# Kernel tuning notes

Measured on AMD Instinct MI355X. Metric: run time of the kernel, lower is better.

## Reference

```python
import jax, jax.numpy as jnp
import numpy as np

B, S, D, K = 16384, 50, 512, 5  # batch, pred_horizon(=steps), dec_units, components_n
H = S  # time_stamp width equals pred_horizon


def setup_inputs() -> dict:
    key = jax.random.key(0)
    ks = jax.random.split(key, 13)
    sc = 0.05
    f32 = jnp.float32
    return {
        "conditions": jax.random.normal(ks[0], (B, S, 3), f32),
        "state_h": jax.random.normal(ks[1], (B, D), f32),
        "state_c": jax.random.normal(ks[2], (B, D), f32),
        # merger LSTM (input = enc_h[D] ++ cond[3])
        "W_m": jax.random.normal(ks[3], (D + 3, 4 * D), f32) * sc,
        "U_m": jax.random.normal(ks[4], (D, 4 * D), f32) * sc,
        "b_m": jnp.zeros((4 * D,), f32),
        # merger MDN heads packed: [alphas|mus_long|sigmas_long|mus_lat|sigmas_lat|rhos]
        "Wh_m": jax.random.normal(ks[5], (D + H, 6 * K), f32) * sc,
        "bh_m": jnp.zeros((6 * K,), f32),
        # yielder LSTM
        "W_y": jax.random.normal(ks[6], (D + 3, 4 * D), f32) * sc,
        "U_y": jax.random.normal(ks[7], (D, 4 * D), f32) * sc,
        "b_y": jnp.zeros((4 * D,), f32),
        # yielder MDN heads packed: [alphas|mus_long|sigmas_long]
        "Wh_y": jax.random.normal(ks[8], (D + H, 3 * K), f32) * sc,
        "bh_y": jnp.zeros((3 * K,), f32),
    }


def _lstm_step(x, h, c, W, U, b):
    # Keras LSTM gate order: i, f, g(cell), o
    z = x @ W + h @ U + b
    i, f, g, o = jnp.split(z, 4, axis=-1)
    c2 = jax.nn.sigmoid(f) * c + jax.nn.sigmoid(i) * jnp.tanh(g)
    h2 = jax.nn.sigmoid(o) * jnp.tanh(c2)
    return h2, c2


def reference(conditions, state_h, state_c, W_m, U_m, b_m, Wh_m, bh_m,
              W_y, U_y, b_y, Wh_y, bh_y):
    # time_stamp[s] = ones in [:s+1] (lower-triangular)
    time_stamp = jnp.tril(jnp.ones((S, H), conditions.dtype))
    enc_h = state_h  # re-fed every step, [B, D]
    # With teacher_percent=1.0 both merger and yielder step conditions are
    # conditions[:, t, :3] at step t (step 0 also uses t=0).
    conds_t = jnp.transpose(conditions, (1, 0, 2))  # [S, B, 3]

    def step(carry, xs):
        h_m, c_m, h_y, c_y = carry
        cond_t, ts = xs  # [B,3], [H]
        x_in = jnp.concatenate([enc_h, cond_t], axis=-1)  # [B, D+3]
        ts_b = jnp.broadcast_to(ts, (h_m.shape[0], H))
        # merger vehicle
        h_m, c_m = _lstm_step(x_in, h_m, c_m, W_m, U_m, b_m)
        feat_m = jnp.concatenate([h_m, ts_b], axis=-1)  # [B, D+H]
        zm = feat_m @ Wh_m + bh_m
        a, ml, sl, mlt, slt, r = jnp.split(zm, 6, axis=-1)
        pm = jnp.concatenate([jax.nn.softmax(a, axis=-1), ml, jnp.exp(sl),
                              mlt, jnp.exp(slt), jnp.tanh(r)], axis=-1)  # [B,30]
        # yielder vehicle
        h_y, c_y = _lstm_step(x_in, h_y, c_y, W_y, U_y, b_y)
        feat_y = jnp.concatenate([h_y, ts_b], axis=-1)
        zy = feat_y @ Wh_y + bh_y
        ay, mly, sly = jnp.split(zy, 3, axis=-1)
        py = jnp.concatenate([jax.nn.softmax(ay, axis=-1), mly, jnp.exp(sly)], axis=-1)  # [B,15]
        return (h_m, c_m, h_y, c_y), (pm, py)

    carry0 = (state_h, state_c, state_h, state_c)
    _, (param_m, param_y) = jax.lax.scan(step, carry0, (conds_t, time_stamp))
    param_m = jnp.transpose(param_m, (1, 0, 2))  # [B, S, 30]
    param_y = jnp.transpose(param_y, (1, 0, 2))  # [B, S, 15]
    return param_m, param_y
```

## Files before the change

### kernel.cpp

```cpp
#include <hip/hip_runtime.h>

typedef __bf16 bf16;
typedef __attribute__((ext_vector_type(8))) __bf16 bf16x8;
typedef __attribute__((ext_vector_type(4))) __bf16 bf16x4;
typedef __attribute__((ext_vector_type(4))) float f32x4;
typedef __attribute__((ext_vector_type(4))) int i32x4;

#define B_TOT 16384
#define SEQ 50
#define DH 512
#define ZW 2048
#define NT 16

#define MFMA16(a, b, c) __builtin_amdgcn_mfma_f32_16x16x32_bf16(a, b, c, 0, 0, 0)

__device__ __forceinline__ float fsigm(float x) {
    return __fdividef(1.0f, 1.0f + __expf(-x));
}
__device__ __forceinline__ float ftanh(float x) {
    float e = __expf(2.0f * x);
    return 1.0f - __fdividef(2.0f, e + 1.0f);
}

__device__ __forceinline__ void gload16(const bf16* g, void* l) {
    __builtin_amdgcn_global_load_lds(
        (const __attribute__((address_space(1))) unsigned int*)g,
        (__attribute__((address_space(3))) unsigned int*)l, 16, 0, 0);
}


__global__ void init_state(const float* __restrict__ sh, const float* __restrict__ sc,
                           bf16* __restrict__ h0m, bf16* __restrict__ h0y,
                           float* __restrict__ cm, float* __restrict__ cy) {
    size_t i = (size_t)blockIdx.x * 256 + threadIdx.x;
    float v = sh[i];
    bf16 hb = (bf16)v;
    h0m[i] = hb;
    h0y[i] = hb;
    float c = sc[i];
    cm[i] = c;
    cy[i] = c;
}

__device__ __forceinline__ int orig_col(int colp) {
    return ((colp >> 4) & 3) * 512 + ((colp >> 6) << 4) + (colp & 15);
}

__global__ void reorder_weights(const float* __restrict__ Um, const float* __restrict__ Uy,
                                const float* __restrict__ Wm, const float* __restrict__ Wy,
                                bf16* __restrict__ UtM, bf16* __restrict__ UtY,
                                bf16* __restrict__ WtM, bf16* __restrict__ WtY) {
    int idx = blockIdx.x * 256 + threadIdx.x;
    int which = idx >> 20;
    int r = idx & ((1 << 20) - 1);
    int colp = r >> 9, k = r & 511;
    int orig = orig_col(colp);
    const float* src = which == 0 ? Um : which == 1 ? Uy : which == 2 ? Wm : Wy;
    bf16* dst = which == 0 ? UtM : which == 1 ? UtY : which == 2 ? WtM : WtY;
    int cb = colp >> 4, fr = colp & 15;
    int kt = k >> 5, fq = (k >> 3) & 3, e = k & 7;
    int lane = fq * 16 + fr;
    dst[(((size_t)(cb * 16 + kt) * 64 + lane) << 3) + e] = (bf16)src[(size_t)k * ZW + orig];
}

__global__ void build_wc2(const float* __restrict__ Wm, const float* __restrict__ Wy,
                          float* __restrict__ Wc2M, float* __restrict__ Wc2Y) {
    int idx = blockIdx.x * 256 + threadIdx.x;
    if (idx >= 2 * 512 * 12) return;
    int which = idx / 6144;
    int r2 = idx % 6144;
    int hcol = r2 / 12, rg = r2 % 12;
    int r = rg >> 2, g = rg & 3;
    const float* src = which ? Wy : Wm;
    float* dst = which ? Wc2Y : Wc2M;
    dst[hcol * 12 + rg] = src[(size_t)(512 + r) * ZW + g * 512 + hcol];
}

__global__ void cond_transpose(const float* __restrict__ cond, float* __restrict__ condT4) {
    int idx = blockIdx.x * 256 + threadIdx.x;
    if (idx >= SEQ * B_TOT) return;
    int t = idx / B_TOT, row = idx % B_TOT;
    const float* s = cond + ((size_t)row * SEQ + t) * 3;
    f32x4 v = {s[0], s[1], s[2], 0.f};
    *(f32x4*)(condT4 + (size_t)idx * 4) = v;
}

__global__ void build_heads(const float* __restrict__ Whm, const float* __restrict__ bhm,
                            const float* __restrict__ Why, const float* __restrict__ bhy,
                            bf16* __restrict__ WhmT, bf16* __restrict__ WhyT,
                            float* __restrict__ tscm, float* __restrict__ tscy) {
    int i = blockIdx.x * 256 + threadIdx.x;
    const int N1 = 32 * 512, N2 = 16 * 512, N3 = SEQ * 32, N4 = SEQ * 16;
    if (i < N1) {
        int n = i >> 9, k = i & 511;
        WhmT[i] = (bf16)(n < 30 ? Whm[k * 30 + n] : 0.f);
    } else if (i < N1 + N2) {
        int j = i - N1;
        int n = j >> 9, k = j & 511;
        WhyT[j] = (bf16)(n < 15 ? Why[k * 15 + n] : 0.f);
    } else if (i < N1 + N2 + N3) {
        int j = i - (N1 + N2);
        int tt = j >> 5, col = j & 31;
        float v = 0.f;
        if (col < 30) {
            v = bhm[col];
            for (int s = 0; s <= tt; ++s) v += Whm[(512 + s) * 30 + col];
        }
        tscm[j] = v;
    } else if (i < N1 + N2 + N3 + N4) {
        int j = i - (N1 + N2 + N3);
        int tt = j >> 4, col = j & 15;
        float v = 0.f;
        if (col < 15) {
            v = bhy[col];
            for (int s = 0; s <= tt; ++s) v += Why[(512 + s) * 15 + col];
        }
        tscy[j] = v;
    }
}


#define FENCE() asm volatile("" ::: "memory")
#define BARRIER()                        \
    do {                                 \
        FENCE();                         \
        __builtin_amdgcn_s_barrier();    \
        FENCE();                         \
    } while (0)
#define WAIT_LGKM0()                                          \
    do {                                                      \
        asm volatile("s_waitcnt lgkmcnt(0)" ::: "memory");    \
        __builtin_amdgcn_sched_barrier(0);                    \
    } while (0)
#define WAIT_VM(n)                                                  \
    do {                                                            \
        asm volatile("s_waitcnt vmcnt(" #n ")" ::: "memory");       \
        __builtin_amdgcn_sched_barrier(0);                          \
    } while (0)

template <int MODE>
__global__ __launch_bounds__(256, 3) void gemm_step(
    const bf16* __restrict__ Am, const bf16* __restrict__ Ay,
    const bf16* __restrict__ BtM, const bf16* __restrict__ BtY,
    const bf16* __restrict__ xwM, const bf16* __restrict__ xwY,
    const float* __restrict__ Wc2M, const float* __restrict__ Wc2Y,
    const float* __restrict__ biasM, const float* __restrict__ biasY,
    float* __restrict__ cM, float* __restrict__ cY,
    bf16* __restrict__ hoM, bf16* __restrict__ hoY,
    bf16* __restrict__ xoM, bf16* __restrict__ xoY,
    const float* __restrict__ condT4, int t) {
    __shared__ bf16 As[3][128][32];

    const int tid = threadIdx.x;
    const int wave = tid >> 6, lane = tid & 63;
    const int brow = blockIdx.x * 128, ncb = blockIdx.y * 128;
    const int bz = blockIdx.z;
    const bf16* A = bz ? Ay : Am;
    const bf16* Bt = bz ? BtY : BtM;

    const int fr = lane & 15, fq = lane >> 4;
    const int wr = wave >> 1, wc = wave & 1;

    const int srow = tid >> 2;
    const int sc8 = (((tid & 3) ^ ((srow >> 1) & 3)) << 3);
    const bf16* Asrc = A + (size_t)(brow + srow) * DH + sc8;
    char* stA = (char*)As + wave * 1024;

    const int cxor = ((fq ^ ((fr >> 1) & 3)) << 4);
    const char* Ard = (char*)As + (wr * 64 + fr) * 64 + cxor;

    const uint64_t bbase =
        (uint64_t)(const char*)Bt + (uint64_t)(blockIdx.y * 8 + wc * 4) * 16384 + lane * 16;

    f32x4 acc[4][4];
#pragma unroll
    for (int m = 0; m < 4; ++m)
#pragma unroll
        for (int n = 0; n < 4; ++n) acc[m][n] = (f32x4){0.f, 0.f, 0.f, 0.f};

    i32x4 bgbuf[2][4];

#define STAGE(slot, kts)                                    \
    do {                                                    \
        const bf16* _s = Asrc + (kts) * 32;                 \
        char* _d = stA + (slot) * 8192;                     \
        gload16(_s, _d);                                    \
        gload16(_s + 64 * DH, _d + 4096);                   \
    } while (0)

#define BGLOAD(bank, kts)                                                        \
    do {                                                                         \
        uint64_t _a = bbase + (uint64_t)(kts) * 1024;                            \
        asm volatile("global_load_dwordx4 %0, %1, off"                          \
                     : "=&v"(bgbuf[bank][0]) : "v"(_a) : "memory");              \
        asm volatile("global_load_dwordx4 %0, %1, off"                          \
                     : "=&v"(bgbuf[bank][1]) : "v"(_a + 16384) : "memory");      \
        asm volatile("global_load_dwordx4 %0, %1, off"                          \
                     : "=&v"(bgbuf[bank][2]) : "v"(_a + 32768) : "memory");      \
        asm volatile("global_load_dwordx4 %0, %1, off"                          \
                     : "=&v"(bgbuf[bank][3]) : "v"(_a + 49152) : "memory");      \
    } while (0)

    BGLOAD(0, 0);
    STAGE(0, 0);
    STAGE(1, 1);
    WAIT_VM(2);
    BARRIER();

#pragma unroll
    for (int kt = 0; kt < NT - 1; ++kt) {
        const int rcur = kt % 3;
        STAGE((kt + 2) % 3, (kt + 2 < NT) ? kt + 2 : NT - 1);
        BGLOAD((kt + 1) & 1, kt + 1);
        bf16x8 af[4];
        {
            const char* _a = Ard + rcur * 8192;
            af[0] = *(const bf16x8*)(_a);
            af[1] = *(const bf16x8*)(_a + 1024);
            af[2] = *(const bf16x8*)(_a + 2048);
            af[3] = *(const bf16x8*)(_a + 3072);
        }
        WAIT_LGKM0();
        WAIT_VM(6);
        __builtin_amdgcn_s_setprio(1);
#pragma unroll
        for (int m = 0; m < 4; ++m)
#pragma unroll
            for (int n = 0; n < 4; ++n)
                acc[m][n] = MFMA16(af[m], __builtin_bit_cast(bf16x8, bgbuf[kt & 1][n]),
                                   acc[m][n]);
        __builtin_amdgcn_s_setprio(0);
        __builtin_amdgcn_sched_barrier(0);
        BARRIER();
    }
    {
        bf16x8 af[4];
        const char* _a = Ard + ((NT - 1) % 3) * 8192;
        af[0] = *(const bf16x8*)(_a);
        af[1] = *(const bf16x8*)(_a + 1024);
        af[2] = *(const bf16x8*)(_a + 2048);
        af[3] = *(const bf16x8*)(_a + 3072);
        WAIT_LGKM0();
        WAIT_VM(0);
        __builtin_amdgcn_s_setprio(1);
#pragma unroll
        for (int m = 0; m < 4; ++m)
#pragma unroll
            for (int n = 0; n < 4; ++n)
                acc[m][n] = MFMA16(af[m], __builtin_bit_cast(bf16x8, bgbuf[(NT - 1) & 1][n]),
                                   acc[m][n]);
        __builtin_amdgcn_s_setprio(0);
        __builtin_amdgcn_sched_barrier(0);
    }

    const int jb = blockIdx.y * 2 + wc;
    const int hcol = jb * 16 + fr;
    const int rowbase = brow + wr * 64 + fq * 4;

    if (MODE == 0) {
        const float* bias = bz ? biasY : biasM;
        bf16* XO = bz ? xoY : xoM;
#pragma unroll
        for (int m = 0; m < 4; ++m)
#pragma unroll
            for (int j = 0; j < 4; ++j) {
                const int row = rowbase + m * 16 + j;
                bf16x4 v;
#pragma unroll
                for (int n = 0; n < 4; ++n) v[n] = (bf16)(acc[m][n][j] + bias[n * 512 + hcol]);
                *(bf16x4*)(XO + (size_t)row * ZW + hcol * 4) = v;
            }
    } else {
        float* Cb = bz ? cY : cM;
        bf16* Ho = bz ? hoY : hoM;
        const bf16* xw = bz ? xwY : xwM;
        const float* Wc2 = bz ? Wc2Y : Wc2M;
        f32x4 wcv0 = *(const f32x4*)(Wc2 + hcol * 12);
        f32x4 wcv1 = *(const f32x4*)(Wc2 + hcol * 12 + 4);
        f32x4 wcv2 = *(const f32x4*)(Wc2 + hcol * 12 + 8);
        bf16x4 xwv[4][4];
        float cv[4][4];
#pragma unroll
        for (int m = 0; m < 4; ++m)
#pragma unroll
            for (int j = 0; j < 4; ++j) {
                const int row = rowbase + m * 16 + j;
                xwv[m][j] = *(const bf16x4*)(xw + (size_t)row * ZW + hcol * 4);
                cv[m][j] = Cb[(size_t)row * DH + hcol];
            }
#pragma unroll
        for (int m = 0; m < 4; ++m) {
            f32x4 cd[4];
#pragma unroll
            for (int j = 0; j < 4; ++j)
                cd[j] = *(const f32x4*)(condT4 + ((size_t)t * B_TOT + rowbase + m * 16 + j) * 4);
#pragma unroll
            for (int j = 0; j < 4; ++j) {
                float z[4];
#pragma unroll
                for (int g = 0; g < 4; ++g)
                    z[g] = acc[m][g][j] + (float)xwv[m][j][g] + cd[j][0] * wcv0[g] +
                           cd[j][1] * wcv1[g] + cd[j][2] * wcv2[g];
                float ii = fsigm(z[0]);
                float ff = fsigm(z[1]);
                float gg = ftanh(z[2]);
                float oo = fsigm(z[3]);
                const int row = rowbase + m * 16 + j;
                size_t ci = (size_t)row * DH + hcol;
                float cn = ff * cv[m][j] + ii * gg;
                Cb[ci] = cn;
                Ho[ci] = (bf16)(oo * ftanh(cn));
            }
        }
    }
#undef STAGE
#undef BGLOAD
}

__global__ __launch_bounds__(128) void heads_step(
    const bf16* __restrict__ hm, const bf16* __restrict__ hy,
    const bf16* __restrict__ WhmT, const bf16* __restrict__ WhyT,
    const float* __restrict__ tscm, const float* __restrict__ tscy,
    float* __restrict__ out, int t) {
    __shared__ float zbuf[2 * 768];
    const int tid = threadIdx.x, wave = tid >> 6, lane = tid & 63;
    const int fr = lane & 15, fq = lane >> 4;
    const int rbase = blockIdx.x * 32 + wave * 16;

    f32x4 am0 = {0.f, 0.f, 0.f, 0.f}, am1 = {0.f, 0.f, 0.f, 0.f}, ay0 = {0.f, 0.f, 0.f, 0.f};

    for (int k0 = 0; k0 < DH; k0 += 32) {
        const size_t ao = (size_t)(rbase + fr) * DH + k0 + fq * 8;
        bf16x8 a0 = *(const bf16x8*)(hm + ao);
        bf16x8 y0 = *(const bf16x8*)(hy + ao);
        const size_t bo = (size_t)fr * DH + k0 + fq * 8;
        bf16x8 b0 = *(const bf16x8*)(WhmT + bo);
        bf16x8 b1 = *(const bf16x8*)(WhmT + bo + 16 * DH);
        bf16x8 yb = *(const bf16x8*)(WhyT + bo);
        am0 = MFMA16(a0, b0, am0);
        am1 = MFMA16(a0, b1, am1);
        ay0 = MFMA16(y0, yb, ay0);
    }

    float* zm = zbuf + wave * 768;
    float* zy = zm + 512;
#pragma unroll
    for (int j = 0; j < 4; ++j) {
        int rl = fq * 4 + j;
        zm[rl * 32 + fr] = am0[j] + tscm[t * 32 + fr];
        zm[rl * 32 + 16 + fr] = am1[j] + tscm[t * 32 + 16 + fr];
        zy[rl * 16 + fr] = ay0[j] + tscy[t * 16 + fr];
    }
    __syncthreads();

    const int r = lane & 15;
    const size_t grow = (size_t)rbase + r;
    if (lane < 16) {
        float z[30];
#pragma unroll
        for (int i = 0; i < 30; ++i) z[i] = zm[r * 32 + i];
        float* o = out + (grow * SEQ + t) * 30;
        float mx = z[0];
#pragma unroll
        for (int i = 1; i < 5; ++i) mx = fmaxf(mx, z[i]);
        float e[5], s = 0.f;
#pragma unroll
        for (int i = 0; i < 5; ++i) {
            e[i] = __expf(z[i] - mx);
            s += e[i];
        }
        float inv = __fdividef(1.f, s);
#pragma unroll
        for (int i = 0; i < 5; ++i) o[i] = e[i] * inv;
#pragma unroll
        for (int i = 5; i < 10; ++i) o[i] = z[i];
#pragma unroll
        for (int i = 10; i < 15; ++i) o[i] = __expf(z[i]);
#pragma unroll
        for (int i = 15; i < 20; ++i) o[i] = z[i];
#pragma unroll
        for (int i = 20; i < 25; ++i) o[i] = __expf(z[i]);
#pragma unroll
        for (int i = 25; i < 30; ++i) o[i] = ftanh(z[i]);
    } else if (lane < 32) {
        float z[15];
#pragma unroll
        for (int i = 0; i < 15; ++i) z[i] = zy[r * 16 + i];
        float* o = out + (size_t)B_TOT * SEQ * 30 + (grow * SEQ + t) * 15;
        float mx = z[0];
#pragma unroll
        for (int i = 1; i < 5; ++i) mx = fmaxf(mx, z[i]);
        float e[5], s = 0.f;
#pragma unroll
        for (int i = 0; i < 5; ++i) {
            e[i] = __expf(z[i] - mx);
            s += e[i];
        }
        float inv = __fdividef(1.f, s);
#pragma unroll
        for (int i = 0; i < 5; ++i) o[i] = e[i] * inv;
#pragma unroll
        for (int i = 5; i < 10; ++i) o[i] = z[i];
#pragma unroll
        for (int i = 10; i < 15; ++i) o[i] = __expf(z[i]);
    }
}

extern "C" void kernel_launch(void* const* d_in, const int* in_sizes, int n_in,
                              void* d_out, int out_size, void* d_ws, size_t ws_size,
                              hipStream_t stream) {
    const float* cond = (const float*)d_in[0];
    const float* sh = (const float*)d_in[1];
    const float* sc = (const float*)d_in[2];
    const float* Wm = (const float*)d_in[3];
    const float* Um = (const float*)d_in[4];
    const float* bm = (const float*)d_in[5];
    const float* Whm = (const float*)d_in[6];
    const float* bhm = (const float*)d_in[7];
    const float* Wy = (const float*)d_in[8];
    const float* Uy = (const float*)d_in[9];
    const float* by_ = (const float*)d_in[10];
    const float* Why = (const float*)d_in[11];
    const float* bhy = (const float*)d_in[12];
    float* out = (float*)d_out;

    char* p = (char*)d_ws;
    auto take = [&](size_t bytes) {
        char* r = p;
        p += (bytes + 255) & ~(size_t)255;
        return r;
    };
    bf16* UtM = (bf16*)take((size_t)ZW * DH * 2);
    bf16* UtY = (bf16*)take((size_t)ZW * DH * 2);
    bf16* WtM = (bf16*)take((size_t)ZW * DH * 2);
    bf16* WtY = (bf16*)take((size_t)ZW * DH * 2);
    float* Wc2M = (float*)take(512 * 12 * 4);
    float* Wc2Y = (float*)take(512 * 12 * 4);
    bf16* WhmT = (bf16*)take(32 * DH * 2);
    bf16* WhyT = (bf16*)take(16 * DH * 2);
    float* tscm = (float*)take(SEQ * 32 * 4);
    float* tscy = (float*)take(SEQ * 16 * 4);
    float* condT4 = (float*)take((size_t)SEQ * B_TOT * 4 * 4);
    bf16* xwM = (bf16*)take((size_t)B_TOT * ZW * 2);
    bf16* xwY = (bf16*)take((size_t)B_TOT * ZW * 2);
    bf16* hM0 = (bf16*)take((size_t)B_TOT * DH * 2);
    bf16* hM1 = (bf16*)take((size_t)B_TOT * DH * 2);
    bf16* hY0 = (bf16*)take((size_t)B_TOT * DH * 2);
    bf16* hY1 = (bf16*)take((size_t)B_TOT * DH * 2);
    float* cMb = (float*)take((size_t)B_TOT * DH * 4);
    float* cYb = (float*)take((size_t)B_TOT * DH * 4);
    bf16* hM[2] = {hM0, hM1};
    bf16* hY[2] = {hY0, hY1};

    init_state<<<(B_TOT * DH) / 256, 256, 0, stream>>>(sh, sc, hM0, hY0, cMb, cYb);
    reorder_weights<<<(4 * ZW * DH) / 256, 256, 0, stream>>>(Um, Uy, Wm, Wy, UtM, UtY, WtM, WtY);
    build_wc2<<<(2 * 512 * 12 + 255) / 256, 256, 0, stream>>>(Wm, Wy, Wc2M, Wc2Y);
    cond_transpose<<<(SEQ * B_TOT + 255) / 256, 256, 0, stream>>>(cond, condT4);
    build_heads<<<(32 * 512 + 16 * 512 + SEQ * 32 + SEQ * 16 + 255) / 256, 256, 0, stream>>>(
        Whm, bhm, Why, bhy, WhmT, WhyT, tscm, tscy);

    dim3 ggrid(B_TOT / 128, ZW / 128, 2);
    gemm_step<0><<<ggrid, 256, 0, stream>>>(hM0, hM0, WtM, WtY, nullptr, nullptr,
                                            nullptr, nullptr, bm, by_, nullptr, nullptr,
                                            nullptr, nullptr, xwM, xwY, condT4, 0);

    for (int t = 0; t < SEQ; ++t) {
        const int a = t & 1, b = (t + 1) & 1;
        gemm_step<1><<<ggrid, 256, 0, stream>>>(hM[a], hY[a], UtM, UtY, xwM, xwY,
                                                Wc2M, Wc2Y, nullptr, nullptr, cMb, cYb,
                                                hM[b], hY[b], nullptr, nullptr, condT4, t);
        heads_step<<<B_TOT / 32, 128, 0, stream>>>(hM[b], hY[b], WhmT, WhyT, tscm, tscy, out, t);
    }
}
```

Baseline: 7.943 ms.

## Transpose cell state and xW buffers to column-major, remap blocks per XCD

Stores the cell-state buffer and the precomputed input projection column-major (per hidden column, contiguous over batch), so each lane's epilogue reads and writes 16-byte vectors instead of scattered scalars. A new transpose kernel initializes the cell state in that layout. Block indices are remapped so consecutive blocks on the same XCD share batch rows for L2 reuse. Launch bounds raised to 4 waves per SIMD, which may force register spilling.

```diff
diff --git a/kernel.cpp b/kernel.cpp
--- a/kernel.cpp
+++ b/kernel.cpp
@@ -29,17 +29,32 @@
 }
 
 
-__global__ void init_state(const float* __restrict__ sh, const float* __restrict__ sc,
-                           bf16* __restrict__ h0m, bf16* __restrict__ h0y,
-                           float* __restrict__ cm, float* __restrict__ cy) {
+__global__ void init_state(const float* __restrict__ sh,
+                           bf16* __restrict__ h0m, bf16* __restrict__ h0y) {
     size_t i = (size_t)blockIdx.x * 256 + threadIdx.x;
-    float v = sh[i];
-    bf16 hb = (bf16)v;
+    bf16 hb = (bf16)sh[i];
     h0m[i] = hb;
     h0y[i] = hb;
-    float c = sc[i];
-    cm[i] = c;
-    cy[i] = c;
+}
+
+__global__ void transpose_c(const float* __restrict__ src,
+                            float* __restrict__ dM, float* __restrict__ dY) {
+    __shared__ float tile[64][65];
+    const int tx = blockIdx.x;
+    const int ty = blockIdx.y;
+    const int lr = threadIdx.x & 63;
+    const int lw = threadIdx.x >> 6;
+#pragma unroll
+    for (int rr = lw; rr < 64; rr += 4)
+        tile[rr][lr] = src[(size_t)(tx * 64 + rr) * DH + ty * 64 + lr];
+    __syncthreads();
+#pragma unroll
+    for (int rr = lw; rr < 64; rr += 4) {
+        float v = tile[lr][rr];
+        size_t o = (size_t)(ty * 64 + rr) * B_TOT + tx * 64 + lr;
+        dM[o] = v;
+        dY[o] = v;
+    }
 }
 
 __device__ __forceinline__ int orig_col(int colp) {
@@ -139,7 +154,7 @@
     } while (0)
 
 template <int MODE>
-__global__ __launch_bounds__(256, 3) void gemm_step(
+__global__ __launch_bounds__(256, 4) void gemm_step(
     const bf16* __restrict__ Am, const bf16* __restrict__ Ay,
     const bf16* __restrict__ BtM, const bf16* __restrict__ BtY,
     const bf16* __restrict__ xwM, const bf16* __restrict__ xwY,
@@ -153,7 +168,11 @@
 
     const int tid = threadIdx.x;
     const int wave = tid >> 6, lane = tid & 63;
-    const int brow = blockIdx.x * 128, ncb = blockIdx.y * 128;
+    const int lin = blockIdx.y * 128 + blockIdx.x;
+    const int xcd = lin & 7, jj = lin >> 3;
+    const int bx = xcd * 16 + (jj >> 4);
+    const int by = jj & 15;
+    const int brow = bx * 128;
     const int bz = blockIdx.z;
     const bf16* A = bz ? Ay : Am;
     const bf16* Bt = bz ? BtY : BtM;
@@ -170,7 +189,7 @@
     const char* Ard = (char*)As + (wr * 64 + fr) * 64 + cxor;
 
     const uint64_t bbase =
-        (uint64_t)(const char*)Bt + (uint64_t)(blockIdx.y * 8 + wc * 4) * 16384 + lane * 16;
+        (uint64_t)(const char*)Bt + (uint64_t)(by * 8 + wc * 4) * 16384 + lane * 16;
 
     f32x4 acc[4][4];
 #pragma unroll
@@ -253,23 +272,37 @@
         __builtin_amdgcn_sched_barrier(0);
     }
 
-    const int jb = blockIdx.y * 2 + wc;
+    const int jb = by * 2 + wc;
     const int hcol = jb * 16 + fr;
     const int rowbase = brow + wr * 64 + fq * 4;
 
     if (MODE == 0) {
         const float* bias = bz ? biasY : biasM;
         bf16* XO = bz ? xoY : xoM;
-#pragma unroll
-        for (int m = 0; m < 4; ++m)
-#pragma unroll
-            for (int j = 0; j < 4; ++j) {
-                const int row = rowbase + m * 16 + j;
-                bf16x4 v;
-#pragma unroll
-                for (int n = 0; n < 4; ++n) v[n] = (bf16)(acc[m][n][j] + bias[n * 512 + hcol]);
-                *(bf16x4*)(XO + (size_t)row * ZW + hcol * 4) = v;
+        float b0 = bias[hcol], b1 = bias[512 + hcol], b2 = bias[1024 + hcol],
+              b3 = bias[1536 + hcol];
+#pragma unroll
+        for (int m = 0; m < 4; ++m) {
+            const int row0 = rowbase + m * 16;
+            bf16x8 v0, v1;
+#pragma unroll
+            for (int j = 0; j < 2; ++j) {
+                v0[j * 4 + 0] = (bf16)(acc[m][0][j] + b0);
+                v0[j * 4 + 1] = (bf16)(acc[m][1][j] + b1);
+                v0[j * 4 + 2] = (bf16)(acc[m][2][j] + b2);
+                v0[j * 4 + 3] = (bf16)(acc[m][3][j] + b3);
             }
+#pragma unroll
+            for (int j = 2; j < 4; ++j) {
+                v1[(j - 2) * 4 + 0] = (bf16)(acc[m][0][j] + b0);
+                v1[(j - 2) * 4 + 1] = (bf16)(acc[m][1][j] + b1);
+                v1[(j - 2) * 4 + 2] = (bf16)(acc[m][2][j] + b2);
+                v1[(j - 2) * 4 + 3] = (bf16)(acc[m][3][j] + b3);
+            }
+            bf16* o = XO + ((size_t)hcol * B_TOT + row0) * 4;
+            *(bf16x8*)(o) = v0;
+            *(bf16x8*)(o + 8) = v1;
+        }
     } else {
         float* Cb = bz ? cY : cM;
         bf16* Ho = bz ? hoY : hoM;
@@ -278,39 +311,36 @@
         f32x4 wcv0 = *(const f32x4*)(Wc2 + hcol * 12);
         f32x4 wcv1 = *(const f32x4*)(Wc2 + hcol * 12 + 4);
         f32x4 wcv2 = *(const f32x4*)(Wc2 + hcol * 12 + 8);
-        bf16x4 xwv[4][4];
-        float cv[4][4];
-#pragma unroll
-        for (int m = 0; m < 4; ++m)
-#pragma unroll
-            for (int j = 0; j < 4; ++j) {
-                const int row = rowbase + m * 16 + j;
-                xwv[m][j] = *(const bf16x4*)(xw + (size_t)row * ZW + hcol * 4);
-                cv[m][j] = Cb[(size_t)row * DH + hcol];
-            }
 #pragma unroll
         for (int m = 0; m < 4; ++m) {
+            const int row0 = rowbase + m * 16;
+            const bf16* xp = xw + ((size_t)hcol * B_TOT + row0) * 4;
+            bf16x8 xv0 = *(const bf16x8*)(xp);
+            bf16x8 xv1 = *(const bf16x8*)(xp + 8);
+            f32x4 cvm = *(const f32x4*)(Cb + (size_t)hcol * B_TOT + row0);
             f32x4 cd[4];
 #pragma unroll
             for (int j = 0; j < 4; ++j)
-                cd[j] = *(const f32x4*)(condT4 + ((size_t)t * B_TOT + rowbase + m * 16 + j) * 4);
+                cd[j] = *(const f32x4*)(condT4 + ((size_t)t * B_TOT + row0 + j) * 4);
+            f32x4 cnew;
 #pragma unroll
             for (int j = 0; j < 4; ++j) {
                 float z[4];
 #pragma unroll
-                for (int g = 0; g < 4; ++g)
-                    z[g] = acc[m][g][j] + (float)xwv[m][j][g] + cd[j][0] * wcv0[g] +
-                           cd[j][1] * wcv1[g] + cd[j][2] * wcv2[g];
+                for (int g = 0; g < 4; ++g) {
+                    float xwv = (j < 2) ? (float)xv0[j * 4 + g] : (float)xv1[(j - 2) * 4 + g];
+                    z[g] = acc[m][g][j] + xwv + cd[j][0] * wcv0[g] + cd[j][1] * wcv1[g] +
+                           cd[j][2] * wcv2[g];
+                }
                 float ii = fsigm(z[0]);
                 float ff = fsigm(z[1]);
                 float gg = ftanh(z[2]);
                 float oo = fsigm(z[3]);
-                const int row = rowbase + m * 16 + j;
-                size_t ci = (size_t)row * DH + hcol;
-                float cn = ff * cv[m][j] + ii * gg;
-                Cb[ci] = cn;
-                Ho[ci] = (bf16)(oo * ftanh(cn));
+                float cn = ff * cvm[j] + ii * gg;
+                cnew[j] = cn;
+                Ho[(size_t)(row0 + j) * DH + hcol] = (bf16)(oo * ftanh(cn));
             }
+            *(f32x4*)(Cb + (size_t)hcol * B_TOT + row0) = cnew;
         }
     }
 #undef STAGE
@@ -452,7 +482,8 @@
     bf16* hM[2] = {hM0, hM1};
     bf16* hY[2] = {hY0, hY1};
 
-    init_state<<<(B_TOT * DH) / 256, 256, 0, stream>>>(sh, sc, hM0, hY0, cMb, cYb);
+    init_state<<<(B_TOT * DH) / 256, 256, 0, stream>>>(sh, hM0, hY0);
+    transpose_c<<<dim3(B_TOT / 64, DH / 64), 256, 0, stream>>>(sc, cMb, cYb);
     reorder_weights<<<(4 * ZW * DH) / 256, 256, 0, stream>>>(Um, Uy, Wm, Wy, UtM, UtY, WtM, WtY);
     build_wc2<<<(2 * 512 * 12 + 255) / 256, 256, 0, stream>>>(Wm, Wy, Wc2M, Wc2Y);
     cond_transpose<<<(SEQ * B_TOT + 255) / 256, 256, 0, stream>>>(cond, condT4);
```

After: 8.001 ms. Within noise of the previous version (+0.7%).
